# Optimization experiments

Measured on AMD Instinct MI355X. Metric: run time of the kernel, lower is better.

The kernel has to match this reference:

```python
import jax, jax.numpy as jnp
import numpy as np

N = 4096      # batch (e.g. nodes)
MUL = 128     # multiplicity of every irrep chunk
INV_SQRT3 = 1.0 / float(np.sqrt(3.0))  # CG norm for 1x1->0 and 0x1->1 / 1x0->1
INV_SQRT6 = 1.0 / float(np.sqrt(6.0))  # CG norm for 1x1->1 (Levi-Civita / sqrt(6))

# Levi-Civita tensor eps[i,j,k]
_EPS = np.zeros((3, 3, 3), dtype=np.float32)
for a, b, c in [(0, 1, 2), (1, 2, 0), (2, 0, 1)]:
    _EPS[a, b, c] = 1.0
    _EPS[a, c, b] = -1.0
EPS = jnp.asarray(_EPS)


def setup_inputs() -> dict:
    key = jax.random.key(0)
    ks = jax.random.split(key, 9)
    # e3nn path normalization folded into weight init std:
    # std = 1/sqrt(mul1*mul2*num_paths_into_that_output_irrep)
    std2 = 1.0 / float(np.sqrt(MUL * MUL * 2))  # scalar out: 2 paths
    std3 = 1.0 / float(np.sqrt(MUL * MUL * 3))  # vector out: 3 paths
    W = (MUL, MUL, MUL)
    return {
        "x1_s": jax.random.normal(ks[0], (N, MUL), dtype=jnp.float32),
        "x1_v": jax.random.normal(ks[1], (N, MUL, 3), dtype=jnp.float32),
        "x2_s": jax.random.normal(ks[2], (N, MUL), dtype=jnp.float32),
        "x2_v": jax.random.normal(ks[3], (N, MUL, 3), dtype=jnp.float32),
        "w_sss": jax.random.normal(ks[4], W, dtype=jnp.float32) * std2,
        "w_vvs": jax.random.normal(ks[5], W, dtype=jnp.float32) * std2,
        "w_svv": jax.random.normal(ks[6], W, dtype=jnp.float32) * std3,
        "w_vsv": jax.random.normal(ks[7], W, dtype=jnp.float32) * std3,
        "w_vvv": jax.random.normal(ks[8], W, dtype=jnp.float32) * std3,
    }


def reference(x1_s, x1_v, x2_s, x2_v, w_sss, w_vvs, w_svv, w_vsv, w_vvv):
    # ---- paths into 0e (scalar) output ----
    # 0e x 0e -> 0e : CG = 1
    a = jnp.einsum('nu,uvw->nvw', x1_s, w_sss)           # [N,MUL,MUL]
    out_s = jnp.einsum('nvw,nv->nw', a, x2_s)            # [N,MUL]
    # 1o x 1o -> 0e : CG = delta_ij / sqrt(3)
    dot = jnp.einsum('nui,nvi->nuv', x1_v, x2_v) * INV_SQRT3
    out_s = out_s + jnp.einsum('nuv,uvw->nw', dot, w_vvs)
    # ---- paths into 1o (vector) output ----
    # 0e x 1o -> 1o : CG = delta / sqrt(3)
    b = jnp.einsum('nu,uvw->nvw', x1_s, w_svv)
    out_v = jnp.einsum('nvw,nvk->nwk', b, x2_v) * INV_SQRT3   # [N,MUL,3]
    # 1o x 0e -> 1o : CG = delta / sqrt(3)
    c = jnp.einsum('nv,uvw->nuw', x2_s, w_vsv)
    out_v = out_v + jnp.einsum('nuw,nuk->nwk', c, x1_v) * INV_SQRT3
    # 1o x 1o -> 1o : CG = eps_ijk / sqrt(6)  (cross product)
    c1 = jnp.einsum('nvj,ijk->nvik', x2_v, EPS)               # [N,MUL,3,3]
    cross = jnp.einsum('nui,nvik->nuvk', x1_v, c1)            # [N,MUL,MUL,3]
    out_v = out_v + jnp.einsum('nuvk,uvw->nwk', cross, w_vvv) * INV_SQRT6
    # pack IrrepsArray 128x0e+128x1o as flat [N, 128 + 384]
    return jnp.concatenate([out_s, out_v.reshape(out_v.shape[0], -1)], axis=-1)
```

## Files before the change

### kernel.cpp

```cpp
#include <hip/hip_runtime.h>
#include <hip/hip_bf16.h>


typedef _Float16 f16;
typedef _Float16 f16x8 __attribute__((ext_vector_type(8)));
typedef _Float16 h2 __attribute__((ext_vector_type(2)));
typedef float f32x4 __attribute__((ext_vector_type(4)));
typedef unsigned u32;

#define WT_BYTES  (5u*4u*128u*4096u*2u)
#define X1_BYTES  (32u*4u*16384u*2u)
#define SLICE_EL  655360u
#define CHUNK_EL  5120u

__device__ __forceinline__ h2 bc(u32 x){ union{u32 u; h2 h;} c; c.u=x; return c.h; }

union F8 { h2 h[4]; f16x8 v; };

__device__ __forceinline__ void gl_lds16(const f16* g, f16* l) {
    __builtin_amdgcn_global_load_lds(
        (const __attribute__((address_space(1))) void*)g,
        (__attribute__((address_space(3))) void*)l,
        16, 0, 0);
}

__global__ __launch_bounds__(256) void pack_w_kernel(
    const float* __restrict__ w0, const float* __restrict__ w1,
    const float* __restrict__ w2, const float* __restrict__ w3,
    const float* __restrict__ w4, f16* __restrict__ wt)
{
    __shared__ float tl[64][130];
    const int b = blockIdx.x;
    const int p = b >> 7;
    const int u = b & 127;
    const int usec = u >> 5;
    const int uin  = u & 31;
    const float* src = (p==0)?w0:(p==1)?w1:(p==2)?w2:(p==3)?w3:w4;
    const float scale = (p==0)?1.0f:(p==4)?0.40824829046386302f:0.57735026918962576f;

    for (int h = 0; h < 2; ++h) {
        const float* spR = src + (size_t)u*16384 + (size_t)h*8192;
        #pragma unroll
        for (int k = 0; k < 8; ++k) {
            const int e4 = (k*256 + threadIdx.x) * 4;
            const float4 v4 = *(const float4*)(spR + e4);
            const int vi = e4 >> 7, w = e4 & 127;
            tl[vi][w+0]=v4.x; tl[vi][w+1]=v4.y; tl[vi][w+2]=v4.z; tl[vi][w+3]=v4.w;
        }
        __syncthreads();
        #pragma unroll
        for (int k = 0; k < 4; ++k) {
            const int cid = k*256 + threadIdx.x;
            const int vbh  = cid >> 9;
            const int wsec = (cid >> 7) & 3;
            const int w    = (cid >> 2) & 31;
            const int q    = cid & 3;
            const int vb   = h*2 + vbh;
            const int c    = vb*32 + uin;
            const int qs   = q ^ ((w >> 1) & 3);
            f16x8 t8;
            #pragma unroll
            for (int j = 0; j < 8; ++j)
                t8[j] = (f16)(tl[vbh*32 + q*8 + j][wsec*32 + w] * scale);
            *(f16x8*)(wt + (size_t)(usec*4 + wsec)*SLICE_EL + (size_t)c*CHUNK_EL
                          + p*1024 + w*32 + qs*8) = t8;
        }
        __syncthreads();
    }
}

__global__ __launch_bounds__(256) void pack_x_kernel(
    const float* __restrict__ x1s, const float* __restrict__ x1v,
    const float* __restrict__ x2s, const float* __restrict__ x2v,
    f16* __restrict__ x1g, f16* __restrict__ x2g)
{
    if (blockIdx.x < 128) {
        __shared__ uint2 tl[128][33];
        const int nb = blockIdx.x;
        #pragma unroll
        for (int k = 0; k < 16; ++k) {
            const int idx = k*256 + threadIdx.x;
            const int u = idx & 127, nd = idx >> 7;
            const size_t i = (size_t)(nb*32 + nd)*128 + u;
            union { f16 h[4]; uint2 u2; } tp;
            tp.h[0] = (f16)x1s[i];
            tp.h[1] = (f16)x1v[i*3 + 0];
            tp.h[2] = (f16)x1v[i*3 + 1];
            tp.h[3] = (f16)x1v[i*3 + 2];
            tl[u][nd] = tp.u2;
        }
        __syncthreads();
        uint2* og = (uint2*)x1g;
        const int t = nb >> 2, nd0 = (nb & 3) * 32;
        #pragma unroll
        for (int k = 0; k < 16; ++k) {
            const int idx = k*256 + threadIdx.x;
            const int u = idx >> 5, nd = idx & 31;
            og[(((t*4 + (u>>5))*32 + (u&31)) << 7) + nd0 + nd] = tl[u][nd];
        }
    } else {
        const int tt = (blockIdx.x - 128)*256 + threadIdx.x;
        const int n = tt >> 7, v = tt & 127;
        const size_t b = (size_t)n*512;
        const size_t i = (size_t)n*128 + v;
        x2g[b +   0 + v] = (f16)x2s[i];
        x2g[b + 128 + v] = (f16)x2v[i*3 + 0];
        x2g[b + 256 + v] = (f16)x2v[i*3 + 1];
        x2g[b + 384 + v] = (f16)x2v[i*3 + 2];
    }
}

__global__ __launch_bounds__(256, 2) void tp_main(
    const f16* __restrict__ wt, const f16* __restrict__ x1g,
    const f16* __restrict__ x2g, float* __restrict__ out)
{
    __shared__ __align__(16) f16 wlds[4*CHUNK_EL];
    __shared__ __align__(16) f16 x1lds[16384];

    const int tid  = threadIdx.x;
    const int lane = tid & 63;
    const int wv   = tid >> 6;
    const int kg   = lane >> 4;
    const int lr   = lane & 15;

    const int b    = blockIdx.x;
    const int s    = (b & 7)*2 + ((b >> 3) & 1);
    const int t    = b >> 4;
    const int usec = s >> 2;
    const int wsec = s & 3;

    const f16* wstream = wt + (size_t)s * SLICE_EL;

    int boff[2];
    #pragma unroll
    for (int ct = 0; ct < 2; ++ct) {
        const int wp = ct*16 + lr;
        boff[ct] = wp*32 + ((kg ^ ((wp >> 1) & 3)) * 8);
    }

    {
        const f16* src = x1g + ((size_t)(t*4 + usec) << 14);
        #pragma unroll
        for (int r = 0; r < 8; ++r)
            gl_lds16(src + r*2048 + tid*8, x1lds + r*2048 + wv*512 + lane*8);
    }
    #pragma unroll
    for (int k = 0; k < 2; ++k) {
        const f16* sc = wstream + k*CHUNK_EL + wv*1280 + lane*8;
        f16* dc = wlds + k*CHUNK_EL + wv*1280;
        gl_lds16(sc, dc);
        gl_lds16(sc + 512, dc + 512);
        if (lane < 32) gl_lds16(sc + 1024, dc + 1024);
    }
    __syncthreads();

    f32x4 acc[2][2][4];
    #pragma unroll
    for (int rt = 0; rt < 2; ++rt)
        #pragma unroll
        for (int c2 = 0; c2 < 2; ++c2)
            #pragma unroll
            for (int d = 0; d < 4; ++d)
                acc[rt][c2][d] = (f32x4){0.f, 0.f, 0.f, 0.f};

    h2 xq[2][4][4];
    const f16* wsrc = wstream + 2*CHUNK_EL + wv*1280 + lane*8;

    for (int vb = 0; vb < 4; ++vb) {
        #pragma unroll
        for (int rt = 0; rt < 2; ++rt) {
            const int n = t*128 + wv*32 + rt*16 + lr;
            const f16* xb = x2g + ((size_t)n << 9) + kg*8 + vb*32;
            #pragma unroll
            for (int q = 0; q < 4; ++q) {
                const uint4 h = *(const uint4*)(xb + (q << 7));
                xq[rt][q][0] = bc(h.x); xq[rt][q][1] = bc(h.y);
                xq[rt][q][2] = bc(h.z); xq[rt][q][3] = bc(h.w);
            }
        }
        for (int u2b = 0; u2b < 32; u2b += 4) {
            #pragma unroll
            for (int uu = 0; uu < 4; ++uu) {
                const int u2 = u2b + uu;
                const int c  = vb*32 + u2;

                if (c < 126) {
                    f16* dc = wlds + ((uu + 2) & 3)*CHUNK_EL + wv*1280;
                    gl_lds16(wsrc, dc);
                    gl_lds16(wsrc + 512, dc + 512);
                    if (lane < 32) gl_lds16(wsrc + 1024, dc + 1024);
                }
                wsrc += CHUNK_EL;

                if (u2 == 0 || c == 126) { asm volatile("s_waitcnt vmcnt(3)" ::: "memory"); }
                else if (c == 127)       { asm volatile("s_waitcnt vmcnt(0)" ::: "memory"); }
                else                     { asm volatile("s_waitcnt vmcnt(6)" ::: "memory"); }
                __builtin_amdgcn_s_barrier();
                __builtin_amdgcn_sched_barrier(0);

                f16x8 bfr[5][2];
                const f16* wb = wlds + uu*CHUNK_EL;
                #pragma unroll
                for (int p = 0; p < 5; ++p)
                    #pragma unroll
                    for (int ct = 0; ct < 2; ++ct)
                        bfr[p][ct] = *(const f16x8*)(wb + p*1024 + boff[ct]);

                #pragma unroll
                for (int rt = 0; rt < 2; ++rt) {
                    const uint2 h1 = *(const uint2*)(x1lds + u2*512 + (wv*32 + rt*16 + lr)*4);
                    const h2 ps1 = bc(__builtin_amdgcn_perm(h1.x, h1.x, 0x01000100u));
                    h2 pv[3];
                    pv[0] = bc(__builtin_amdgcn_perm(h1.x, h1.x, 0x03020302u));
                    pv[1] = bc(__builtin_amdgcn_perm(h1.y, h1.y, 0x01000100u));
                    pv[2] = bc(__builtin_amdgcn_perm(h1.y, h1.y, 0x03020302u));

                    {
                        F8 f0, f1;
                        #pragma unroll
                        for (int j = 0; j < 4; ++j) {
                            f0.h[j] = ps1 * xq[rt][0][j];
                            h2 d = pv[0] * xq[rt][1][j];
                            d = __builtin_elementwise_fma(pv[1], xq[rt][2][j], d);
                            f1.h[j] = __builtin_elementwise_fma(pv[2], xq[rt][3][j], d);
                        }
                        #pragma unroll
                        for (int ct = 0; ct < 2; ++ct) {
                            acc[rt][ct][0] = __builtin_amdgcn_mfma_f32_16x16x32_f16(f0.v, bfr[0][ct], acc[rt][ct][0], 0,0,0);
                            acc[rt][ct][0] = __builtin_amdgcn_mfma_f32_16x16x32_f16(f1.v, bfr[1][ct], acc[rt][ct][0], 0,0,0);
                        }
                    }
                    #pragma unroll
                    for (int k = 0; k < 3; ++k) {
                        const int k1 = (k+1) % 3, k2 = (k+2) % 3;
                        F8 fa, fb, fc;
                        #pragma unroll
                        for (int j = 0; j < 4; ++j) {
                            fa.h[j] = ps1   * xq[rt][1+k][j];
                            fb.h[j] = pv[k] * xq[rt][0][j];
                            h2 tx = pv[k1] * xq[rt][1+k2][j];
                            fc.h[j] = __builtin_elementwise_fma(-pv[k2], xq[rt][1+k1][j], tx);
                        }
                        #pragma unroll
                        for (int ct = 0; ct < 2; ++ct) {
                            acc[rt][ct][1+k] = __builtin_amdgcn_mfma_f32_16x16x32_f16(fa.v, bfr[2][ct], acc[rt][ct][1+k], 0,0,0);
                            acc[rt][ct][1+k] = __builtin_amdgcn_mfma_f32_16x16x32_f16(fb.v, bfr[3][ct], acc[rt][ct][1+k], 0,0,0);
                            acc[rt][ct][1+k] = __builtin_amdgcn_mfma_f32_16x16x32_f16(fc.v, bfr[4][ct], acc[rt][ct][1+k], 0,0,0);
                        }
                    }
                }
            }
        }
    }

    #pragma unroll
    for (int rt = 0; rt < 2; ++rt) {
        #pragma unroll
        for (int ct = 0; ct < 2; ++ct) {
            const int w = wsec*32 + ct*16 + lr;
            #pragma unroll
            for (int j = 0; j < 4; ++j) {
                const int n = t*128 + wv*32 + rt*16 + kg*4 + j;
                float* op = out + (size_t)n*512;
                unsafeAtomicAdd(op + w,             acc[rt][ct][0][j]);
                unsafeAtomicAdd(op + 128 + w*3 + 0, acc[rt][ct][1][j]);
                unsafeAtomicAdd(op + 128 + w*3 + 1, acc[rt][ct][2][j]);
                unsafeAtomicAdd(op + 128 + w*3 + 2, acc[rt][ct][3][j]);
            }
        }
    }
}

extern "C" void kernel_launch(void* const* d_in, const int* in_sizes, int n_in,
                              void* d_out, int out_size, void* d_ws, size_t ws_size,
                              hipStream_t stream)
{
    const float* x1s = (const float*)d_in[0];
    const float* x1v = (const float*)d_in[1];
    const float* x2s = (const float*)d_in[2];
    const float* x2v = (const float*)d_in[3];
    const float* w0  = (const float*)d_in[4];
    const float* w1  = (const float*)d_in[5];
    const float* w2  = (const float*)d_in[6];
    const float* w3  = (const float*)d_in[7];
    const float* w4  = (const float*)d_in[8];

    f16* wtb = (f16*)d_ws;
    f16* x1g = (f16*)((char*)d_ws + WT_BYTES);
    f16* x2g = (f16*)((char*)d_ws + WT_BYTES + X1_BYTES);
    float* out = (float*)d_out;

    pack_w_kernel<<<640, 256, 0, stream>>>(w0, w1, w2, w3, w4, wtb);
    pack_x_kernel<<<2176, 256, 0, stream>>>(x1s, x1v, x2s, x2v, x1g, x2g);
    hipMemsetAsync(d_out, 0, (size_t)out_size*sizeof(float), stream);
    tp_main<<<512, 256, 0, stream>>>(wtb, x1g, x2g, out);
}
```

Measured before the change: 239.7 us.

## Retile main kernel to 64-node x 64-output tiles with double-buffered weight chunks

Changes the block tile from 128 nodes x 32 outputs (16 slices) to 64 nodes x 64 outputs (8 slices), repacking weights and x1 accordingly. Each wave now handles one 16-node row tile against four 16-wide column tiles, so x1-derived A fragments are built once per u and reused across four weight column tiles. Weight staging goes from a 4-deep ring with graded vmcnt waits to a 2-deep double buffer with a full vmcnt(0) wait and barrier before issuing the next load. This lowers LDS use and the per-wave A-fragment VALU work, but exposes more global-to-LDS load latency per step.

```diff
diff --git a/kernel.cpp b/kernel.cpp
--- a/kernel.cpp
+++ b/kernel.cpp
@@ -9,9 +9,9 @@
 typedef unsigned u32;
 
 #define WT_BYTES  (5u*4u*128u*4096u*2u)
-#define X1_BYTES  (32u*4u*16384u*2u)
-#define SLICE_EL  655360u
-#define CHUNK_EL  5120u
+#define X1_BYTES  (64u*4u*8192u*2u)
+#define SLICE_EL  1310720u
+#define CHUNK_EL  10240u
 
 __device__ __forceinline__ h2 bc(u32 x){ union{u32 u; h2 h;} c; c.u=x; return c.h; }
 
@@ -51,19 +51,20 @@
         #pragma unroll
         for (int k = 0; k < 4; ++k) {
             const int cid = k*256 + threadIdx.x;
-            const int vbh  = cid >> 9;
-            const int wsec = (cid >> 7) & 3;
-            const int w    = (cid >> 2) & 31;
-            const int q    = cid & 3;
-            const int vb   = h*2 + vbh;
-            const int c    = vb*32 + uin;
-            const int qs   = q ^ ((w >> 1) & 3);
+            const int q     = cid & 3;
+            const int wg    = (cid >> 2) & 127;
+            const int vbh   = cid >> 9;
+            const int vb    = h*2 + vbh;
+            const int c     = vb*32 + uin;
+            const int whalf = wg >> 6;
+            const int wl    = wg & 63;
+            const int qs    = q ^ ((wl >> 1) & 3);
             f16x8 t8;
             #pragma unroll
             for (int j = 0; j < 8; ++j)
-                t8[j] = (f16)(tl[vbh*32 + q*8 + j][wsec*32 + w] * scale);
-            *(f16x8*)(wt + (size_t)(usec*4 + wsec)*SLICE_EL + (size_t)c*CHUNK_EL
-                          + p*1024 + w*32 + qs*8) = t8;
+                t8[j] = (f16)(tl[vbh*32 + q*8 + j][wg] * scale);
+            *(f16x8*)(wt + (size_t)(usec*2 + whalf)*SLICE_EL + (size_t)c*CHUNK_EL
+                          + p*2048 + wl*32 + qs*8) = t8;
         }
         __syncthreads();
     }
@@ -91,12 +92,12 @@
         }
         __syncthreads();
         uint2* og = (uint2*)x1g;
-        const int t = nb >> 2, nd0 = (nb & 3) * 32;
+        const int t = nb >> 1, nd0 = (nb & 1) * 32;
         #pragma unroll
         for (int k = 0; k < 16; ++k) {
             const int idx = k*256 + threadIdx.x;
             const int u = idx >> 5, nd = idx & 31;
-            og[(((t*4 + (u>>5))*32 + (u&31)) << 7) + nd0 + nd] = tl[u][nd];
+            og[(((t*4 + (u>>5))*32 + (u&31)) << 6) + nd0 + nd] = tl[u][nd];
         }
     } else {
         const int tt = (blockIdx.x - 128)*256 + threadIdx.x;
@@ -114,8 +115,8 @@
     const f16* __restrict__ wt, const f16* __restrict__ x1g,
     const f16* __restrict__ x2g, float* __restrict__ out)
 {
-    __shared__ __align__(16) f16 wlds[4*CHUNK_EL];
-    __shared__ __align__(16) f16 x1lds[16384];
+    __shared__ __align__(16) f16 wlds[2*CHUNK_EL];
+    __shared__ __align__(16) f16 x1lds[8192];
 
     const int tid  = threadIdx.x;
     const int lane = tid & 63;
@@ -123,130 +124,115 @@
     const int kg   = lane >> 4;
     const int lr   = lane & 15;
 
-    const int b    = blockIdx.x;
-    const int s    = (b & 7)*2 + ((b >> 3) & 1);
-    const int t    = b >> 4;
-    const int usec = s >> 2;
-    const int wsec = s & 3;
-
-    const f16* wstream = wt + (size_t)s * SLICE_EL;
-
-    int boff[2];
-    #pragma unroll
-    for (int ct = 0; ct < 2; ++ct) {
+    const int b     = blockIdx.x;
+    const int slice = b & 7;
+    const int t     = b >> 3;
+    const int usec  = slice >> 1;
+    const int whalf = slice & 1;
+
+    const f16* wstream = wt + (size_t)slice * SLICE_EL;
+
+    int boff[4];
+    #pragma unroll
+    for (int ct = 0; ct < 4; ++ct) {
         const int wp = ct*16 + lr;
         boff[ct] = wp*32 + ((kg ^ ((wp >> 1) & 3)) * 8);
     }
 
     {
-        const f16* src = x1g + ((size_t)(t*4 + usec) << 14);
-        #pragma unroll
-        for (int r = 0; r < 8; ++r)
-            gl_lds16(src + r*2048 + tid*8, x1lds + r*2048 + wv*512 + lane*8);
-    }
-    #pragma unroll
-    for (int k = 0; k < 2; ++k) {
-        const f16* sc = wstream + k*CHUNK_EL + wv*1280 + lane*8;
-        f16* dc = wlds + k*CHUNK_EL + wv*1280;
-        gl_lds16(sc, dc);
-        gl_lds16(sc + 512, dc + 512);
-        if (lane < 32) gl_lds16(sc + 1024, dc + 1024);
-    }
-    __syncthreads();
-
-    f32x4 acc[2][2][4];
-    #pragma unroll
-    for (int rt = 0; rt < 2; ++rt)
-        #pragma unroll
-        for (int c2 = 0; c2 < 2; ++c2)
+        const f16* src = x1g + ((size_t)(t*4 + usec) << 13);
+        #pragma unroll
+        for (int r = 0; r < 4; ++r)
+            gl_lds16(src + r*2048 + wv*512 + lane*8, x1lds + r*2048 + wv*512 + lane*8);
+    }
+    #pragma unroll
+    for (int r = 0; r < 5; ++r)
+        gl_lds16(wstream + r*2048 + wv*512 + lane*8, wlds + r*2048 + wv*512 + lane*8);
+
+    f32x4 acc[4][4];
+    #pragma unroll
+    for (int c2 = 0; c2 < 4; ++c2)
+        #pragma unroll
+        for (int d = 0; d < 4; ++d)
+            acc[c2][d] = (f32x4){0.f, 0.f, 0.f, 0.f};
+
+    h2 xq[4][4];
+    const f16* wsrc = wstream + CHUNK_EL + wv*512 + lane*8;
+    const f16* x2base = x2g + ((size_t)(t*64 + wv*16 + lr) << 9) + kg*8;
+    const int nodel4 = (wv*16 + lr) * 4;
+
+    for (int vb = 0; vb < 4; ++vb) {
+        {
+            const f16* xb = x2base + vb*32;
+            uint4 h0 = *(const uint4*)(xb);
+            uint4 h1 = *(const uint4*)(xb + 128);
+            uint4 h2v = *(const uint4*)(xb + 256);
+            uint4 h3 = *(const uint4*)(xb + 384);
+            xq[0][0]=bc(h0.x); xq[0][1]=bc(h0.y); xq[0][2]=bc(h0.z); xq[0][3]=bc(h0.w);
+            xq[1][0]=bc(h1.x); xq[1][1]=bc(h1.y); xq[1][2]=bc(h1.z); xq[1][3]=bc(h1.w);
+            xq[2][0]=bc(h2v.x); xq[2][1]=bc(h2v.y); xq[2][2]=bc(h2v.z); xq[2][3]=bc(h2v.w);
+            xq[3][0]=bc(h3.x); xq[3][1]=bc(h3.y); xq[3][2]=bc(h3.z); xq[3][3]=bc(h3.w);
+        }
+        for (int u2b = 0; u2b < 32; u2b += 2) {
             #pragma unroll
-            for (int d = 0; d < 4; ++d)
-                acc[rt][c2][d] = (f32x4){0.f, 0.f, 0.f, 0.f};
-
-    h2 xq[2][4][4];
-    const f16* wsrc = wstream + 2*CHUNK_EL + wv*1280 + lane*8;
-
-    for (int vb = 0; vb < 4; ++vb) {
-        #pragma unroll
-        for (int rt = 0; rt < 2; ++rt) {
-            const int n = t*128 + wv*32 + rt*16 + lr;
-            const f16* xb = x2g + ((size_t)n << 9) + kg*8 + vb*32;
-            #pragma unroll
-            for (int q = 0; q < 4; ++q) {
-                const uint4 h = *(const uint4*)(xb + (q << 7));
-                xq[rt][q][0] = bc(h.x); xq[rt][q][1] = bc(h.y);
-                xq[rt][q][2] = bc(h.z); xq[rt][q][3] = bc(h.w);
-            }
-        }
-        for (int u2b = 0; u2b < 32; u2b += 4) {
-            #pragma unroll
-            for (int uu = 0; uu < 4; ++uu) {
+            for (int uu = 0; uu < 2; ++uu) {
                 const int u2 = u2b + uu;
                 const int c  = vb*32 + u2;
 
-                if (c < 126) {
-                    f16* dc = wlds + ((uu + 2) & 3)*CHUNK_EL + wv*1280;
-                    gl_lds16(wsrc, dc);
-                    gl_lds16(wsrc + 512, dc + 512);
-                    if (lane < 32) gl_lds16(wsrc + 1024, dc + 1024);
-                }
-                wsrc += CHUNK_EL;
-
-                if (u2 == 0 || c == 126) { asm volatile("s_waitcnt vmcnt(3)" ::: "memory"); }
-                else if (c == 127)       { asm volatile("s_waitcnt vmcnt(0)" ::: "memory"); }
-                else                     { asm volatile("s_waitcnt vmcnt(6)" ::: "memory"); }
+                asm volatile("s_waitcnt vmcnt(0)" ::: "memory");
                 __builtin_amdgcn_s_barrier();
                 __builtin_amdgcn_sched_barrier(0);
 
-                f16x8 bfr[5][2];
+                if (c < 127) {
+                    f16* dc = wlds + (uu^1)*CHUNK_EL + wv*512;
+                    #pragma unroll
+                    for (int r = 0; r < 5; ++r)
+                        gl_lds16(wsrc + r*2048, dc + r*2048 + lane*8);
+                }
+                wsrc += CHUNK_EL;
+
+                const uint2 h1 = *(const uint2*)(x1lds + u2*256 + nodel4);
+                const h2 ps1 = bc(__builtin_amdgcn_perm(h1.x, h1.x, 0x01000100u));
+                h2 pv[3];
+                pv[0] = bc(__builtin_amdgcn_perm(h1.x, h1.x, 0x03020302u));
+                pv[1] = bc(__builtin_amdgcn_perm(h1.y, h1.y, 0x01000100u));
+                pv[2] = bc(__builtin_amdgcn_perm(h1.y, h1.y, 0x03020302u));
+
+                F8 f0, f1, fa[3], fb[3], fc[3];
+                #pragma unroll
+                for (int j = 0; j < 4; ++j) {
+                    f0.h[j] = ps1 * xq[0][j];
+                    h2 d = pv[0] * xq[1][j];
+                    d = __builtin_elementwise_fma(pv[1], xq[2][j], d);
+                    f1.h[j] = __builtin_elementwise_fma(pv[2], xq[3][j], d);
+                }
+                #pragma unroll
+                for (int k = 0; k < 3; ++k) {
+                    const int k1 = (k+1) % 3, k2 = (k+2) % 3;
+                    #pragma unroll
+                    for (int j = 0; j < 4; ++j) {
+                        fa[k].h[j] = ps1   * xq[1+k][j];
+                        fb[k].h[j] = pv[k] * xq[0][j];
+                        h2 tx = pv[k1] * xq[1+k2][j];
+                        fc[k].h[j] = __builtin_elementwise_fma(-pv[k2], xq[1+k1][j], tx);
+                    }
+                }
+
                 const f16* wb = wlds + uu*CHUNK_EL;
                 #pragma unroll
-                for (int p = 0; p < 5; ++p)
-                    #pragma unroll
-                    for (int ct = 0; ct < 2; ++ct)
-                        bfr[p][ct] = *(const f16x8*)(wb + p*1024 + boff[ct]);
-
-                #pragma unroll
-                for (int rt = 0; rt < 2; ++rt) {
-                    const uint2 h1 = *(const uint2*)(x1lds + u2*512 + (wv*32 + rt*16 + lr)*4);
-                    const h2 ps1 = bc(__builtin_amdgcn_perm(h1.x, h1.x, 0x01000100u));
-                    h2 pv[3];
-                    pv[0] = bc(__builtin_amdgcn_perm(h1.x, h1.x, 0x03020302u));
-                    pv[1] = bc(__builtin_amdgcn_perm(h1.y, h1.y, 0x01000100u));
-                    pv[2] = bc(__builtin_amdgcn_perm(h1.y, h1.y, 0x03020302u));
-
-                    {
-                        F8 f0, f1;
-                        #pragma unroll
-                        for (int j = 0; j < 4; ++j) {
-                            f0.h[j] = ps1 * xq[rt][0][j];
-                            h2 d = pv[0] * xq[rt][1][j];
-                            d = __builtin_elementwise_fma(pv[1], xq[rt][2][j], d);
-                            f1.h[j] = __builtin_elementwise_fma(pv[2], xq[rt][3][j], d);
-                        }
-                        #pragma unroll
-                        for (int ct = 0; ct < 2; ++ct) {
-                            acc[rt][ct][0] = __builtin_amdgcn_mfma_f32_16x16x32_f16(f0.v, bfr[0][ct], acc[rt][ct][0], 0,0,0);
-                            acc[rt][ct][0] = __builtin_amdgcn_mfma_f32_16x16x32_f16(f1.v, bfr[1][ct], acc[rt][ct][0], 0,0,0);
-                        }
-                    }
+                for (int ct = 0; ct < 4; ++ct) {
+                    f16x8 b0 = *(const f16x8*)(wb +    0 + boff[ct]);
+                    f16x8 b1 = *(const f16x8*)(wb + 2048 + boff[ct]);
+                    f16x8 b2 = *(const f16x8*)(wb + 4096 + boff[ct]);
+                    f16x8 b3 = *(const f16x8*)(wb + 6144 + boff[ct]);
+                    f16x8 b4 = *(const f16x8*)(wb + 8192 + boff[ct]);
+                    acc[ct][0] = __builtin_amdgcn_mfma_f32_16x16x32_f16(f0.v, b0, acc[ct][0], 0,0,0);
+                    acc[ct][0] = __builtin_amdgcn_mfma_f32_16x16x32_f16(f1.v, b1, acc[ct][0], 0,0,0);
                     #pragma unroll
                     for (int k = 0; k < 3; ++k) {
-                        const int k1 = (k+1) % 3, k2 = (k+2) % 3;
-                        F8 fa, fb, fc;
-                        #pragma unroll
-                        for (int j = 0; j < 4; ++j) {
-                            fa.h[j] = ps1   * xq[rt][1+k][j];
-                            fb.h[j] = pv[k] * xq[rt][0][j];
-                            h2 tx = pv[k1] * xq[rt][1+k2][j];
-                            fc.h[j] = __builtin_elementwise_fma(-pv[k2], xq[rt][1+k1][j], tx);
-                        }
-                        #pragma unroll
-                        for (int ct = 0; ct < 2; ++ct) {
-                            acc[rt][ct][1+k] = __builtin_amdgcn_mfma_f32_16x16x32_f16(fa.v, bfr[2][ct], acc[rt][ct][1+k], 0,0,0);
-                            acc[rt][ct][1+k] = __builtin_amdgcn_mfma_f32_16x16x32_f16(fb.v, bfr[3][ct], acc[rt][ct][1+k], 0,0,0);
-                            acc[rt][ct][1+k] = __builtin_amdgcn_mfma_f32_16x16x32_f16(fc.v, bfr[4][ct], acc[rt][ct][1+k], 0,0,0);
-                        }
+                        acc[ct][1+k] = __builtin_amdgcn_mfma_f32_16x16x32_f16(fa[k].v, b2, acc[ct][1+k], 0,0,0);
+                        acc[ct][1+k] = __builtin_amdgcn_mfma_f32_16x16x32_f16(fb[k].v, b3, acc[ct][1+k], 0,0,0);
+                        acc[ct][1+k] = __builtin_amdgcn_mfma_f32_16x16x32_f16(fc[k].v, b4, acc[ct][1+k], 0,0,0);
                     }
                 }
             }
@@ -254,19 +240,16 @@
     }
 
     #pragma unroll
-    for (int rt = 0; rt < 2; ++rt) {
-        #pragma unroll
-        for (int ct = 0; ct < 2; ++ct) {
-            const int w = wsec*32 + ct*16 + lr;
-            #pragma unroll
-            for (int j = 0; j < 4; ++j) {
-                const int n = t*128 + wv*32 + rt*16 + kg*4 + j;
-                float* op = out + (size_t)n*512;
-                unsafeAtomicAdd(op + w,             acc[rt][ct][0][j]);
-                unsafeAtomicAdd(op + 128 + w*3 + 0, acc[rt][ct][1][j]);
-                unsafeAtomicAdd(op + 128 + w*3 + 1, acc[rt][ct][2][j]);
-                unsafeAtomicAdd(op + 128 + w*3 + 2, acc[rt][ct][3][j]);
-            }
+    for (int ct = 0; ct < 4; ++ct) {
+        const int w = whalf*64 + ct*16 + lr;
+        #pragma unroll
+        for (int j = 0; j < 4; ++j) {
+            const int n = t*64 + wv*16 + kg*4 + j;
+            float* op = out + (size_t)n*512;
+            unsafeAtomicAdd(op + w,             acc[ct][0][j]);
+            unsafeAtomicAdd(op + 128 + w*3 + 0, acc[ct][1][j]);
+            unsafeAtomicAdd(op + 128 + w*3 + 1, acc[ct][2][j]);
+            unsafeAtomicAdd(op + 128 + w*3 + 2, acc[ct][3][j]);
         }
     }
 }
```

New measurement: 234.1 us. 1.02x faster.
